# Optimization experiments

Hardware: AMD Instinct MI355X
Metric: run time of the kernel (lower is better)

The kernel has to match this reference:

```python
import jax, jax.numpy as jnp
import numpy as np

H = 512  # hidden_size


def setup_inputs() -> dict:
    key = jax.random.key(0)
    ks = jax.random.split(key, 12)
    B, E, S, V = 64, 512, 400, 50000
    s = 1.0 / np.sqrt(H)
    inp = {
        'embedded': jax.random.normal(ks[0], (B, E), jnp.float32),
        'hidden': jax.random.normal(ks[1], (1, B, H), jnp.float32),
        'encoder_states': jax.random.normal(ks[2], (S, B, H), jnp.float32),
        # GRU params (PyTorch layout: gates ordered r,z,n)
        'w_ih': jax.random.uniform(ks[3], (3 * H, E), jnp.float32, -s, s),
        'w_hh': jax.random.uniform(ks[4], (3 * H, H), jnp.float32, -s, s),
        'b_ih': jax.random.uniform(ks[5], (3 * H,), jnp.float32, -s, s),
        'b_hh': jax.random.uniform(ks[6], (3 * H,), jnp.float32, -s, s),
        # nn.Bilinear(H, H, 1)
        'bilin_w': jax.random.uniform(ks[7], (1, H, H), jnp.float32, -s, s),
        'bilin_b': jax.random.uniform(ks[8], (1,), jnp.float32, -s, s),
        # out: Linear(2H, V)
        'out_w': jax.random.uniform(ks[9], (V, 2 * H), jnp.float32, -1.0 / np.sqrt(2 * H), 1.0 / np.sqrt(2 * H)),
        'out_b': jax.random.uniform(ks[10], (V,), jnp.float32, -1.0 / np.sqrt(2 * H), 1.0 / np.sqrt(2 * H)),
    }
    return inp


def reference(embedded, hidden, encoder_states, w_ih, w_hh, b_ih, b_hh,
              bilin_w, bilin_b, out_w, out_b):
    h0 = hidden[0]                                   # [B, H]
    # --- single-step GRU cell (PyTorch gate order r, z, n) ---
    gi = embedded @ w_ih.T + b_ih                    # [B, 3H]
    gh = h0 @ w_hh.T + b_hh                          # [B, 3H]
    r = jax.nn.sigmoid(gi[:, :H] + gh[:, :H])
    z = jax.nn.sigmoid(gi[:, H:2 * H] + gh[:, H:2 * H])
    n = jnp.tanh(gi[:, 2 * H:] + r * gh[:, 2 * H:])
    h_new = (1.0 - z) * n + z * h0                   # [B, H]
    # --- bilinear attention: energy[s,b] = h_new[b] @ W @ enc[s,b] + bias ---
    tmp = h_new @ bilin_w[0]                         # [B, H]
    energy = jnp.einsum('bh,sbh->sb', tmp, encoder_states) + bilin_b[0]  # [S, B]
    attn = jax.nn.softmax(energy, axis=0)            # softmax over source positions
    context = jnp.einsum('sb,sbh->bh', attn, encoder_states)             # [B, H]
    combined = jnp.concatenate([h_new, context], axis=1)                 # [B, 2H]
    logits = combined @ out_w.T + out_b              # [B, V]
    logp = jax.nn.log_softmax(logits, axis=1)
    return logp, h_new[None], attn[:, :, None]
```

## Files before the change

### kernel.cpp

```cpp
#include <hip/hip_runtime.h>
#include <math.h>

static constexpr int H = 512;
static constexpr int B = 64;
static constexpr int FP = 8;

typedef __bf16 bf16x8 __attribute__((ext_vector_type(8)));
typedef __bf16 bf16x4 __attribute__((ext_vector_type(4)));
typedef float f32x4 __attribute__((ext_vector_type(4)));

__device__ __forceinline__ float sigmoidf_(float x) { return 1.f / (1.f + expf(-x)); }

__global__ __launch_bounds__(256) void gemm_gigh(
    const float* __restrict__ embedded, const float* __restrict__ hidden,
    const float* __restrict__ w_ih, const float* __restrict__ w_hh,
    float* __restrict__ gi, float* __restrict__ gh, int K, int N)
{
    const float* A = blockIdx.y ? hidden : embedded;
    const float* W = blockIdx.y ? w_hh : w_ih;
    float* C       = blockIdx.y ? gh : gi;

    __shared__ __bf16 As[2][64 * 64];
    __shared__ __bf16 Ws[2][64 * 64];

    const int tid  = threadIdx.x;
    const int lane = tid & 63;
    const int wv   = tid >> 6;
    const int n0   = blockIdx.x * 64;
    const int lrow = tid >> 2;
    const int lq   = tid & 3;

    const float* Aptr = A + (size_t)lrow * K + lq * 16;
    const float* Wptr = W + (size_t)(n0 + lrow) * K + lq * 16;

    f32x4 acc[4] = {};
    float4 ra[4], rw[4];
    #pragma unroll
    for (int i = 0; i < 4; ++i) {
        ra[i] = *(const float4*)(Aptr + 4 * i);
        rw[i] = *(const float4*)(Wptr + 4 * i);
    }

    const int ln = lane & 15;
    const int lk = (lane >> 4) << 3;
    const int NT = K >> 6;

    for (int t = 0; t < NT; ++t) {
        __bf16* a_s = As[t & 1];
        __bf16* w_s = Ws[t & 1];
        #pragma unroll
        for (int i = 0; i < 4; ++i) {
            const int off = ((lrow << 6) + lq * 16 + 4 * i) ^ ((lrow & 7) << 3);
            *(bf16x4*)&a_s[off] = bf16x4{ (__bf16)ra[i].x, (__bf16)ra[i].y, (__bf16)ra[i].z, (__bf16)ra[i].w };
            *(bf16x4*)&w_s[off] = bf16x4{ (__bf16)rw[i].x, (__bf16)rw[i].y, (__bf16)rw[i].z, (__bf16)rw[i].w };
        }
        __syncthreads();
        if (t + 1 < NT) {
            const float* Ap = Aptr + (t + 1) * 64;
            const float* Wp = Wptr + (t + 1) * 64;
            #pragma unroll
            for (int i = 0; i < 4; ++i) {
                ra[i] = *(const float4*)(Ap + 4 * i);
                rw[i] = *(const float4*)(Wp + 4 * i);
            }
        }
        bf16x8 bfrag[2];
        #pragma unroll
        for (int ks = 0; ks < 2; ++ks) {
            const int row = wv * 16 + ln;
            const int off = ((row << 6) + ks * 32 + lk) ^ ((row & 7) << 3);
            bfrag[ks] = *(bf16x8*)&w_s[off];
        }
        #pragma unroll
        for (int m = 0; m < 4; ++m) {
            const int row = m * 16 + ln;
            #pragma unroll
            for (int ks = 0; ks < 2; ++ks) {
                const int off = ((row << 6) + ks * 32 + lk) ^ ((row & 7) << 3);
                bf16x8 afrag = *(bf16x8*)&a_s[off];
                acc[m] = __builtin_amdgcn_mfma_f32_16x16x32_bf16(afrag, bfrag[ks], acc[m], 0, 0, 0);
            }
        }
    }

    const int col = n0 + wv * 16 + ln;
    #pragma unroll
    for (int m = 0; m < 4; ++m) {
        const int rbase = m * 16 + (lane >> 4) * 4;
        #pragma unroll
        for (int j = 0; j < 4; ++j)
            C[(size_t)(rbase + j) * N + col] = acc[m][j];
    }
}

__global__ __launch_bounds__(512) void gru_gates(
    const float* __restrict__ gi, const float* __restrict__ gh,
    const float* __restrict__ b_ih, const float* __restrict__ b_hh,
    const float* __restrict__ h0, float* __restrict__ hnew,
    __bf16* __restrict__ cbf)
{
    const int b = blockIdx.x;
    const int h = threadIdx.x;
    const size_t o = (size_t)b * 3 * H;
    const float r = sigmoidf_(gi[o + h] + gh[o + h] + b_ih[h] + b_hh[h]);
    const float z = sigmoidf_(gi[o + H + h] + gh[o + H + h] + b_ih[H + h] + b_hh[H + h]);
    const float n = tanhf(gi[o + 2 * H + h] + b_ih[2 * H + h]
                          + r * (gh[o + 2 * H + h] + b_hh[2 * H + h]));
    const float hn = (1.f - z) * n + z * h0[(size_t)b * H + h];
    hnew[(size_t)b * H + h] = hn;
    cbf[(size_t)b * 2 * H + h] = (__bf16)hn;
}

__global__ __launch_bounds__(256) void gemm_a64_kn(
    const float* __restrict__ A, const float* __restrict__ W,
    float* __restrict__ C, int K, int N, int ldc)
{
    __shared__ float As[64][68];
    __shared__ float Bs[64][68];
    const int tid = threadIdx.x;
    const int n0 = blockIdx.x * 64;
    const int tv = tid & 15;
    const int tb = tid >> 4;
    const int lrow = tid >> 2;
    const int lk0  = (tid & 3) * 16;

    float acc[4][4] = {{0.f, 0.f, 0.f, 0.f}};

    for (int kc = 0; kc < K; kc += 64) {
        #pragma unroll
        for (int i = 0; i < 4; ++i) {
            const float4 a = *(const float4*)(A + (size_t)lrow * K + kc + lk0 + 4 * i);
            As[lk0 + 4 * i + 0][lrow] = a.x;
            As[lk0 + 4 * i + 1][lrow] = a.y;
            As[lk0 + 4 * i + 2][lrow] = a.z;
            As[lk0 + 4 * i + 3][lrow] = a.w;
        }
        {
            const int v  = tid & 63;
            const int kg = tid >> 6;
            #pragma unroll
            for (int i = 0; i < 16; ++i) {
                const int kk = kg * 16 + i;
                Bs[kk][v] = (n0 + v < N) ? W[(size_t)(kc + kk) * N + n0 + v] : 0.f;
            }
        }
        __syncthreads();
        #pragma unroll 16
        for (int kk = 0; kk < 64; ++kk) {
            const float4 a = *(const float4*)&As[kk][tb * 4];
            const float4 b = *(const float4*)&Bs[kk][tv * 4];
            acc[0][0] += a.x * b.x; acc[0][1] += a.x * b.y; acc[0][2] += a.x * b.z; acc[0][3] += a.x * b.w;
            acc[1][0] += a.y * b.x; acc[1][1] += a.y * b.y; acc[1][2] += a.y * b.z; acc[1][3] += a.y * b.w;
            acc[2][0] += a.z * b.x; acc[2][1] += a.z * b.y; acc[2][2] += a.z * b.z; acc[2][3] += a.z * b.w;
            acc[3][0] += a.w * b.x; acc[3][1] += a.w * b.y; acc[3][2] += a.w * b.z; acc[3][3] += a.w * b.w;
        }
        __syncthreads();
    }
    #pragma unroll
    for (int i = 0; i < 4; ++i) {
        const int bb = tb * 4 + i;
        #pragma unroll
        for (int j = 0; j < 4; ++j) {
            const int n = n0 + tv * 4 + j;
            if (n < N) C[(size_t)bb * ldc + n] = acc[i][j];
        }
    }
}

__global__ __launch_bounds__(256) void flash4(
    const float* __restrict__ tmp, const float* __restrict__ enc,
    const float* __restrict__ bilin_b, float* __restrict__ energy,
    float* __restrict__ ctxp, float* __restrict__ mp, float* __restrict__ lp,
    int S)
{
    const int b  = blockIdx.x;
    const int p  = blockIdx.y;
    const int wv = threadIdx.x >> 6;
    const int ln = threadIdx.x & 63;
    const int chunk = (S + FP - 1) / FP;
    const int s0 = p * chunk;
    int s1 = s0 + chunk; if (s1 > S) s1 = S;
    const int k0 = ln * 8;

    const float4 t0 = *(const float4*)(tmp + (size_t)b * H + k0);
    const float4 t1 = *(const float4*)(tmp + (size_t)b * H + k0 + 4);
    const float bb = bilin_b[0];

    float m = -1e30f, l = 0.f;
    float4 c0 = {0.f, 0.f, 0.f, 0.f}, c1 = {0.f, 0.f, 0.f, 0.f};

    for (int s = s0 + wv; s < s1; s += 4) {
        const float* e = enc + ((size_t)s * B + b) * H + k0;
        const float4 e0 = *(const float4*)(e);
        const float4 e1 = *(const float4*)(e + 4);
        float d = e0.x * t0.x + e0.y * t0.y + e0.z * t0.z + e0.w * t0.w
                + e1.x * t1.x + e1.y * t1.y + e1.z * t1.z + e1.w * t1.w;
        #pragma unroll
        for (int off = 32; off; off >>= 1) d += __shfl_xor(d, off);
        const float E = d + bb;
        if (ln == 0) energy[(size_t)s * B + b] = E;
        const float mn = fmaxf(m, E);
        const float sc = expf(m - mn);
        const float w  = expf(E - mn);
        l = l * sc + w;
        c0.x = c0.x * sc + w * e0.x; c0.y = c0.y * sc + w * e0.y;
        c0.z = c0.z * sc + w * e0.z; c0.w = c0.w * sc + w * e0.w;
        c1.x = c1.x * sc + w * e1.x; c1.y = c1.y * sc + w * e1.y;
        c1.z = c1.z * sc + w * e1.z; c1.w = c1.w * sc + w * e1.w;
        m = mn;
    }

    __shared__ float sctx[4][H];
    __shared__ float sm4[4], sl4[4];
    *(float4*)&sctx[wv][k0]     = c0;
    *(float4*)&sctx[wv][k0 + 4] = c1;
    if (ln == 0) { sm4[wv] = m; sl4[wv] = l; }
    __syncthreads();
    const float bm = fmaxf(fmaxf(sm4[0], sm4[1]), fmaxf(sm4[2], sm4[3]));
    const float s0c = expf(sm4[0] - bm), s1c = expf(sm4[1] - bm);
    const float s2c = expf(sm4[2] - bm), s3c = expf(sm4[3] - bm);
    const float bl = sl4[0] * s0c + sl4[1] * s1c + sl4[2] * s2c + sl4[3] * s3c;
    for (int e = threadIdx.x; e < H; e += 256) {
        const float v = sctx[0][e] * s0c + sctx[1][e] * s1c
                      + sctx[2][e] * s2c + sctx[3][e] * s3c;
        ctxp[((size_t)b * FP + p) * H + e] = v;
    }
    if (threadIdx.x == 0) { mp[b * FP + p] = bm; lp[b * FP + p] = bl; }
}

__global__ __launch_bounds__(256) void attn_combine(
    const float* __restrict__ mp, const float* __restrict__ lp,
    const float* __restrict__ ctxp, const float* __restrict__ energy,
    __bf16* __restrict__ cbf, float* __restrict__ attn, int S)
{
    const int b = blockIdx.x;
    const int t = threadIdx.x;
    __shared__ float sc_[FP];
    __shared__ float sM, sInvL;
    if (t == 0) {
        float M = -1e30f;
        #pragma unroll
        for (int p = 0; p < FP; ++p) M = fmaxf(M, mp[b * FP + p]);
        float L = 0.f;
        #pragma unroll
        for (int p = 0; p < FP; ++p) {
            const float s = expf(mp[b * FP + p] - M);
            sc_[p] = s;
            L += lp[b * FP + p] * s;
        }
        sM = M; sInvL = 1.f / L;
    }
    __syncthreads();
    const float M = sM, invL = sInvL;

    for (int e = t; e < H; e += 256) {
        float acc = 0.f;
        #pragma unroll
        for (int p = 0; p < FP; ++p)
            acc += ctxp[((size_t)b * FP + p) * H + e] * sc_[p];
        cbf[(size_t)b * 2 * H + H + e] = (__bf16)(acc * invL);
    }
    for (int s = t; s < S; s += 256)
        attn[(size_t)s * B + b] = expf(energy[(size_t)s * B + b] - M) * invL;
}

__global__ __launch_bounds__(256) void gemm_big(
    const __bf16* __restrict__ Ab,
    const float* __restrict__ W,
    const float* __restrict__ bias,
    float* __restrict__ C, float* __restrict__ pm, float* __restrict__ ps,
    int K, int N, int ldc)
{
    __shared__ __bf16 As[64 * 256];

    const int tid  = threadIdx.x;
    const int lane = tid & 63;
    const int wv   = tid >> 6;
    const int n0   = blockIdx.x * 64 + wv * 16;
    const int ln   = lane & 15;
    const int lk8  = (lane >> 4) << 3;

    int wr = n0 + ln;
    if (wr > N - 1) wr = N - 1;
    const float* wp = W + (size_t)wr * K + lk8;

    f32x4 acc[4] = {};
    const int NQ = K >> 8;

    for (int q = 0; q < NQ; ++q) {
        __syncthreads();
        #pragma unroll
        for (int i = 0; i < 8; ++i) {
            const int c   = tid + i * 256;
            const int row = c >> 5;
            const int eb  = (c & 31) << 3;
            const bf16x8 v = *(const bf16x8*)(Ab + (size_t)row * K + q * 256 + eb);
            const int off = (row << 8) + (eb ^ ((row & 7) << 3));
            *(bf16x8*)&As[off] = v;
        }
        __syncthreads();
        #pragma unroll
        for (int ks = 0; ks < 8; ++ks) {
            const float4 w0 = *(const float4*)(wp + q * 256 + ks * 32);
            const float4 w1 = *(const float4*)(wp + q * 256 + ks * 32 + 4);
            const bf16x8 bw = { (__bf16)w0.x, (__bf16)w0.y, (__bf16)w0.z, (__bf16)w0.w,
                                (__bf16)w1.x, (__bf16)w1.y, (__bf16)w1.z, (__bf16)w1.w };
            #pragma unroll
            for (int m = 0; m < 4; ++m) {
                const int row = m * 16 + ln;
                const int off = (row << 8) + ((ks * 32 + lk8) ^ ((row & 7) << 3));
                const bf16x8 af = *(const bf16x8*)&As[off];
                acc[m] = __builtin_amdgcn_mfma_f32_16x16x32_bf16(af, bw, acc[m], 0, 0, 0);
            }
        }
    }

    const int col = n0 + ln;
    const float bv = (col < N) ? bias[col] : 0.f;
    __syncthreads();
    float* wmf = (float*)As;
    float* wsf = wmf + 256;

    #pragma unroll
    for (int m = 0; m < 4; ++m) {
        #pragma unroll
        for (int j = 0; j < 4; ++j) {
            const int rr = m * 16 + (lane >> 4) * 4 + j;
            float v = acc[m][j] + bv;
            if (col < N) C[(size_t)rr * ldc + col] = v;
            else v = -1e30f;
            float vm = v;
            #pragma unroll
            for (int off = 8; off; off >>= 1) vm = fmaxf(vm, __shfl_xor(vm, off));
            float e = (col < N) ? expf(v - vm) : 0.f;
            #pragma unroll
            for (int off = 8; off; off >>= 1) e += __shfl_xor(e, off);
            if (ln == 0) {
                wmf[wv * 64 + rr] = vm;
                wsf[wv * 64 + rr] = e;
            }
        }
    }
    __syncthreads();
    if (tid < 64) {
        const float m0 = wmf[tid], m1 = wmf[64 + tid], m2 = wmf[128 + tid], m3 = wmf[192 + tid];
        const float bm = fmaxf(fmaxf(m0, m1), fmaxf(m2, m3));
        const float bs = wsf[tid] * expf(m0 - bm) + wsf[64 + tid] * expf(m1 - bm)
                       + wsf[128 + tid] * expf(m2 - bm) + wsf[192 + tid] * expf(m3 - bm);
        pm[(size_t)tid * gridDim.x + blockIdx.x] = bm;
        ps[(size_t)tid * gridDim.x + blockIdx.x] = bs;
    }
}

__global__ __launch_bounds__(256) void lsm_rowcombine(
    const float* __restrict__ pm, const float* __restrict__ ps,
    float* __restrict__ c, int NB)
{
    const int row = blockIdx.x;
    const int t = threadIdx.x;
    const float* pmr = pm + (size_t)row * NB;
    const float* psr = ps + (size_t)row * NB;
    __shared__ float sm_[4], ss_[4];

    float m = -1e30f;
    for (int i = t; i < NB; i += 256) m = fmaxf(m, pmr[i]);
    #pragma unroll
    for (int off = 32; off; off >>= 1) m = fmaxf(m, __shfl_xor(m, off));
    if ((t & 63) == 0) sm_[t >> 6] = m;
    __syncthreads();
    m = fmaxf(fmaxf(sm_[0], sm_[1]), fmaxf(sm_[2], sm_[3]));

    float s = 0.f;
    for (int i = t; i < NB; i += 256) s += psr[i] * expf(pmr[i] - m);
    #pragma unroll
    for (int off = 32; off; off >>= 1) s += __shfl_xor(s, off);
    if ((t & 63) == 0) ss_[t >> 6] = s;
    __syncthreads();
    if (t == 0) c[row] = m + logf(ss_[0] + ss_[1] + ss_[2] + ss_[3]);
}

__global__ __launch_bounds__(256) void lsm_apply(
    float* __restrict__ logits, const float* __restrict__ c, int V)
{
    const int b = blockIdx.y;
    const int i = blockIdx.x * 256 + threadIdx.x;
    const int V4 = V >> 2;
    if (i >= V4) return;
    float4* row = (float4*)(logits + (size_t)b * V);
    float4 v = row[i];
    const float cb = c[b];
    v.x -= cb; v.y -= cb; v.z -= cb; v.w -= cb;
    row[i] = v;
}

extern "C" void kernel_launch(void* const* d_in, const int* in_sizes, int n_in,
                              void* d_out, int out_size, void* d_ws, size_t ws_size,
                              hipStream_t stream)
{
    const float* embedded = (const float*)d_in[0];
    const float* hidden   = (const float*)d_in[1];
    const float* enc      = (const float*)d_in[2];
    const float* w_ih     = (const float*)d_in[3];
    const float* w_hh     = (const float*)d_in[4];
    const float* b_ih     = (const float*)d_in[5];
    const float* b_hh     = (const float*)d_in[6];
    const float* bilin_w  = (const float*)d_in[7];
    const float* bilin_b  = (const float*)d_in[8];
    const float* out_w    = (const float*)d_in[9];
    const float* out_b    = (const float*)d_in[10];
    float* out = (float*)d_out;

    const int S = in_sizes[2] / (B * H);
    const int V = in_sizes[9] / (2 * H);
    const int NB = (V + 63) / 64;

    float* logp = out;
    float* hnew = out + (size_t)B * V;
    float* attn = hnew + (size_t)B * H;

    float* ws     = (float*)d_ws;
    float* gi     = ws;
    float* gh     = gi + (size_t)B * 3 * H;
    float* tmp    = gh + (size_t)B * 3 * H;
    float* energy = tmp + (size_t)B * H;
    float* ctxp   = energy + (size_t)S * B;
    float* mp     = ctxp + (size_t)B * FP * H;
    float* lp     = mp + (size_t)B * FP;
    float* pm     = lp + (size_t)B * FP;
    float* ps     = pm + (size_t)64 * NB;
    float* cb     = ps + (size_t)64 * NB;
    __bf16* cbf   = (__bf16*)(cb + 64);

    gemm_gigh<<<dim3(24, 2), 256, 0, stream>>>(embedded, hidden, w_ih, w_hh, gi, gh, H, 3 * H);

    gru_gates<<<B, H, 0, stream>>>(gi, gh, b_ih, b_hh, hidden, hnew, cbf);

    gemm_a64_kn<<<H / 64, 256, 0, stream>>>(hnew, bilin_w, tmp, H, H, H);

    flash4<<<dim3(B, FP), 256, 0, stream>>>(tmp, enc, bilin_b, energy, ctxp, mp, lp, S);

    attn_combine<<<B, 256, 0, stream>>>(mp, lp, ctxp, energy, cbf, attn, S);

    gemm_big<<<NB, 256, 0, stream>>>(cbf, out_w, out_b, logp, pm, ps, 2 * H, V, V);

    lsm_rowcombine<<<B, 256, 0, stream>>>(pm, ps, cb, NB);

    lsm_apply<<<dim3((V / 4 + 255) / 256, B), 256, 0, stream>>>(logp, cb, V);
}
```

Measured before the change: 153.2 us.

## Make output GEMM persistent with full A tile in LDS and register-prefetched weights

The vocabulary projection kernel becomes persistent: 256 blocks each load the entire 64x1024 bf16 activation matrix into shared memory once, then loop over output column tiles. Inside each tile the fp32 weight rows are streamed through an 8-deep register ring to keep more global loads in flight. This removes the repeated per-block staging of activations and its barriers, and aims to hide weight-load latency. In exchange it uses 128KB+ LDS per block (occupancy of one block per CU) and many more registers, so latency hiding depends entirely on in-flight loads within one block.

Result: slower. 195.9 us (+27.9%).

```diff
diff --git a/kernel.cpp b/kernel.cpp
--- a/kernel.cpp
+++ b/kernel.cpp
@@ -264,91 +264,102 @@
         attn[(size_t)s * B + b] = expf(energy[(size_t)s * B + b] - M) * invL;
 }
 
-__global__ __launch_bounds__(256) void gemm_big(
+__global__ __launch_bounds__(256, 1) void gemm_big(
     const __bf16* __restrict__ Ab,
     const float* __restrict__ W,
     const float* __restrict__ bias,
     float* __restrict__ C, float* __restrict__ pm, float* __restrict__ ps,
-    int K, int N, int ldc)
-{
-    __shared__ __bf16 As[64 * 256];
+    int N, int ldc, int NB)
+{
+    constexpr int K = 1024;
+    __shared__ __bf16 As[64 * 1024];
+    __shared__ float red[512];
 
     const int tid  = threadIdx.x;
     const int lane = tid & 63;
     const int wv   = tid >> 6;
-    const int n0   = blockIdx.x * 64 + wv * 16;
     const int ln   = lane & 15;
     const int lk8  = (lane >> 4) << 3;
 
-    int wr = n0 + ln;
-    if (wr > N - 1) wr = N - 1;
-    const float* wp = W + (size_t)wr * K + lk8;
-
-    f32x4 acc[4] = {};
-    const int NQ = K >> 8;
-
-    for (int q = 0; q < NQ; ++q) {
-        __syncthreads();
-        #pragma unroll
-        for (int i = 0; i < 8; ++i) {
-            const int c   = tid + i * 256;
-            const int row = c >> 5;
-            const int eb  = (c & 31) << 3;
-            const bf16x8 v = *(const bf16x8*)(Ab + (size_t)row * K + q * 256 + eb);
-            const int off = (row << 8) + (eb ^ ((row & 7) << 3));
-            *(bf16x8*)&As[off] = v;
-        }
-        __syncthreads();
-        #pragma unroll
-        for (int ks = 0; ks < 8; ++ks) {
-            const float4 w0 = *(const float4*)(wp + q * 256 + ks * 32);
-            const float4 w1 = *(const float4*)(wp + q * 256 + ks * 32 + 4);
+    #pragma unroll
+    for (int i = 0; i < 32; ++i) {
+        const int c   = (i << 8) + tid;
+        const int row = c >> 7;
+        const int eb  = (c & 127) << 3;
+        const bf16x8 v = *(const bf16x8*)(Ab + (size_t)row * K + eb);
+        const int off = (row << 10) + (eb ^ ((row & 7) << 3));
+        *(bf16x8*)&As[off] = v;
+    }
+    __syncthreads();
+
+    for (int t = blockIdx.x; t < NB; t += gridDim.x) {
+        const int n0 = t * 64 + wv * 16;
+        int wr = n0 + ln;
+        if (wr > N - 1) wr = N - 1;
+        const float* wq = W + (size_t)wr * K + lk8;
+
+        f32x4 acc[4] = {};
+
+        float4 ring[8][2];
+        #pragma unroll
+        for (int s = 0; s < 8; ++s) {
+            ring[s][0] = *(const float4*)(wq + s * 32);
+            ring[s][1] = *(const float4*)(wq + s * 32 + 4);
+        }
+        #pragma unroll
+        for (int s = 0; s < 32; ++s) {
+            const float4 w0 = ring[s & 7][0];
+            const float4 w1 = ring[s & 7][1];
+            if (s < 24) {
+                ring[s & 7][0] = *(const float4*)(wq + (s + 8) * 32);
+                ring[s & 7][1] = *(const float4*)(wq + (s + 8) * 32 + 4);
+            }
             const bf16x8 bw = { (__bf16)w0.x, (__bf16)w0.y, (__bf16)w0.z, (__bf16)w0.w,
                                 (__bf16)w1.x, (__bf16)w1.y, (__bf16)w1.z, (__bf16)w1.w };
             #pragma unroll
             for (int m = 0; m < 4; ++m) {
                 const int row = m * 16 + ln;
-                const int off = (row << 8) + ((ks * 32 + lk8) ^ ((row & 7) << 3));
+                const int off = (row << 10) + ((s * 32 + lk8) ^ ((row & 7) << 3));
                 const bf16x8 af = *(const bf16x8*)&As[off];
                 acc[m] = __builtin_amdgcn_mfma_f32_16x16x32_bf16(af, bw, acc[m], 0, 0, 0);
             }
         }
-    }
-
-    const int col = n0 + ln;
-    const float bv = (col < N) ? bias[col] : 0.f;
-    __syncthreads();
-    float* wmf = (float*)As;
-    float* wsf = wmf + 256;
-
-    #pragma unroll
-    for (int m = 0; m < 4; ++m) {
-        #pragma unroll
-        for (int j = 0; j < 4; ++j) {
-            const int rr = m * 16 + (lane >> 4) * 4 + j;
-            float v = acc[m][j] + bv;
-            if (col < N) C[(size_t)rr * ldc + col] = v;
-            else v = -1e30f;
-            float vm = v;
+
+        const int col = n0 + ln;
+        const float bv = (col < N) ? bias[col] : 0.f;
+        float* wmf = red;
+        float* wsf = red + 256;
+
+        #pragma unroll
+        for (int m = 0; m < 4; ++m) {
             #pragma unroll
-            for (int off = 8; off; off >>= 1) vm = fmaxf(vm, __shfl_xor(vm, off));
-            float e = (col < N) ? expf(v - vm) : 0.f;
-            #pragma unroll
-            for (int off = 8; off; off >>= 1) e += __shfl_xor(e, off);
-            if (ln == 0) {
-                wmf[wv * 64 + rr] = vm;
-                wsf[wv * 64 + rr] = e;
-            }
-        }
-    }
-    __syncthreads();
-    if (tid < 64) {
-        const float m0 = wmf[tid], m1 = wmf[64 + tid], m2 = wmf[128 + tid], m3 = wmf[192 + tid];
-        const float bm = fmaxf(fmaxf(m0, m1), fmaxf(m2, m3));
-        const float bs = wsf[tid] * expf(m0 - bm) + wsf[64 + tid] * expf(m1 - bm)
-                       + wsf[128 + tid] * expf(m2 - bm) + wsf[192 + tid] * expf(m3 - bm);
-        pm[(size_t)tid * gridDim.x + blockIdx.x] = bm;
-        ps[(size_t)tid * gridDim.x + blockIdx.x] = bs;
+            for (int j = 0; j < 4; ++j) {
+                const int rr = m * 16 + (lane >> 4) * 4 + j;
+                float v = acc[m][j] + bv;
+                if (col < N) C[(size_t)rr * ldc + col] = v;
+                else v = -1e30f;
+                float vm = v;
+                #pragma unroll
+                for (int off = 8; off; off >>= 1) vm = fmaxf(vm, __shfl_xor(vm, off));
+                float e = (col < N) ? expf(v - vm) : 0.f;
+                #pragma unroll
+                for (int off = 8; off; off >>= 1) e += __shfl_xor(e, off);
+                if (ln == 0) {
+                    wmf[wv * 64 + rr] = vm;
+                    wsf[wv * 64 + rr] = e;
+                }
+            }
+        }
+        __syncthreads();
+        if (tid < 64) {
+            const float m0 = wmf[tid], m1 = wmf[64 + tid], m2 = wmf[128 + tid], m3 = wmf[192 + tid];
+            const float bm = fmaxf(fmaxf(m0, m1), fmaxf(m2, m3));
+            const float bs = wsf[tid] * expf(m0 - bm) + wsf[64 + tid] * expf(m1 - bm)
+                           + wsf[128 + tid] * expf(m2 - bm) + wsf[192 + tid] * expf(m3 - bm);
+            pm[(size_t)tid * NB + t] = bm;
+            ps[(size_t)tid * NB + t] = bs;
+        }
+        __syncthreads();
     }
 }
 
@@ -441,7 +452,7 @@
 
     attn_combine<<<B, 256, 0, stream>>>(mp, lp, ctxp, energy, cbf, attn, S);
 
-    gemm_big<<<NB, 256, 0, stream>>>(cbf, out_w, out_b, logp, pm, ps, 2 * H, V, V);
+    gemm_big<<<256, 256, 0, stream>>>(cbf, out_w, out_b, logp, pm, ps, V, V, NB);
 
     lsm_rowcombine<<<B, 256, 0, stream>>>(pm, ps, cb, NB);
 
```

## Stream out_w and activations into LDS via async global_load_lds triple buffering

Applied to the files above, without the earlier changes.

Rewrites the large output-projection GEMM so both the fp32 weight tiles and bf16 activation tiles are copied directly into swizzled LDS with global_load_lds, using a three-stage ring buffer and manual vmcnt waits. Previously each wave read weights straight from global memory inside the MFMA loop and the activations were staged synchronously. The goal is to overlap weight streaming, which dominates this memory-bound kernel, with MFMA compute. In exchange it uses more LDS (about 76KB per block), which may lower occupancy, and it hardcodes K=1024 (4096-byte row stride, 16 phases).

After: 162.0 us. 5.7% more time.

```diff
diff --git a/kernel.cpp b/kernel.cpp
--- a/kernel.cpp
+++ b/kernel.cpp
@@ -10,6 +10,12 @@
 typedef float f32x4 __attribute__((ext_vector_type(4)));
 
 __device__ __forceinline__ float sigmoidf_(float x) { return 1.f / (1.f + expf(-x)); }
+
+__device__ __forceinline__ void gload16(const void* gsrc, void* lds) {
+    __builtin_amdgcn_global_load_lds(
+        (const __attribute__((address_space(1))) unsigned int*)gsrc,
+        (__attribute__((address_space(3))) unsigned int*)lds, 16, 0, 0);
+}
 
 __global__ __launch_bounds__(256) void gemm_gigh(
     const float* __restrict__ embedded, const float* __restrict__ hidden,
@@ -269,57 +275,82 @@
     const float* __restrict__ W,
     const float* __restrict__ bias,
     float* __restrict__ C, float* __restrict__ pm, float* __restrict__ ps,
-    int K, int N, int ldc)
-{
-    __shared__ __bf16 As[64 * 256];
+    int N, int ldc)
+{
+    __shared__ float  Wl[3][64 * 64];
+    __shared__ __bf16 Al[3][64 * 64];
+    __shared__ float  red[512];
 
     const int tid  = threadIdx.x;
     const int lane = tid & 63;
     const int wv   = tid >> 6;
-    const int n0   = blockIdx.x * 64 + wv * 16;
     const int ln   = lane & 15;
-    const int lk8  = (lane >> 4) << 3;
-
-    int wr = n0 + ln;
-    if (wr > N - 1) wr = N - 1;
-    const float* wp = W + (size_t)wr * K + lk8;
+    const int row0 = blockIdx.x * 64;
+
+    const int lane4 = lane >> 4;
+    const int g16   = lane & 15;
+    const int lane8 = lane >> 3;
+    const int g8    = lane & 7;
+    size_t wsrc[4];
+    #pragma unroll
+    for (int i = 0; i < 4; ++i) {
+        const int rl = (wv * 4 + i) * 4 + lane4;
+        int gr = row0 + rl; if (gr > N - 1) gr = N - 1;
+        wsrc[i] = (size_t)gr * 4096 + (size_t)((g16 ^ (rl & 7)) << 4);
+    }
+    size_t asrc[2];
+    #pragma unroll
+    for (int j = 0; j < 2; ++j) {
+        const int rl = (wv * 2 + j) * 8 + lane8;
+        asrc[j] = (size_t)rl * 2048 + (size_t)((g8 ^ (rl & 7)) << 4);
+    }
+    const char* wB = (const char*)W;
+    const char* aB = (const char*)Ab;
+
+    auto stage = [&](int b, int ph) {
+        #pragma unroll
+        for (int i = 0; i < 4; ++i)
+            gload16(wB + wsrc[i] + (size_t)ph * 256, &Wl[b][(wv * 4 + i) * 256]);
+        #pragma unroll
+        for (int j = 0; j < 2; ++j)
+            gload16(aB + asrc[j] + (size_t)ph * 128, &Al[b][(wv * 2 + j) * 512]);
+    };
 
     f32x4 acc[4] = {};
-    const int NQ = K >> 8;
-
-    for (int q = 0; q < NQ; ++q) {
-        __syncthreads();
-        #pragma unroll
-        for (int i = 0; i < 8; ++i) {
-            const int c   = tid + i * 256;
-            const int row = c >> 5;
-            const int eb  = (c & 31) << 3;
-            const bf16x8 v = *(const bf16x8*)(Ab + (size_t)row * K + q * 256 + eb);
-            const int off = (row << 8) + (eb ^ ((row & 7) << 3));
-            *(bf16x8*)&As[off] = v;
-        }
-        __syncthreads();
-        #pragma unroll
-        for (int ks = 0; ks < 8; ++ks) {
-            const float4 w0 = *(const float4*)(wp + q * 256 + ks * 32);
-            const float4 w1 = *(const float4*)(wp + q * 256 + ks * 32 + 4);
+
+    stage(0, 0);
+    stage(1, 1);
+
+    for (int ph = 0; ph < 16; ++ph) {
+        const int b = ph % 3;
+        if (ph + 2 < 16) stage((ph + 2) % 3, ph + 2);
+        if (ph == 15) asm volatile("s_waitcnt vmcnt(0)" ::: "memory");
+        else          asm volatile("s_waitcnt vmcnt(6)" ::: "memory");
+        __builtin_amdgcn_sched_barrier(0);
+        __builtin_amdgcn_s_barrier();
+        #pragma unroll
+        for (int ks = 0; ks < 2; ++ks) {
+            const int r  = wv * 16 + ln;
+            const int G0 = ks * 8 + (lane >> 4) * 2;
+            const float4 w0 = *(const float4*)&Wl[b][r * 64 + (((G0    ) ^ (r & 7)) << 2)];
+            const float4 w1 = *(const float4*)&Wl[b][r * 64 + (((G0 + 1) ^ (r & 7)) << 2)];
             const bf16x8 bw = { (__bf16)w0.x, (__bf16)w0.y, (__bf16)w0.z, (__bf16)w0.w,
                                 (__bf16)w1.x, (__bf16)w1.y, (__bf16)w1.z, (__bf16)w1.w };
+            const int Ga = ks * 4 + (lane >> 4);
             #pragma unroll
             for (int m = 0; m < 4; ++m) {
-                const int row = m * 16 + ln;
-                const int off = (row << 8) + ((ks * 32 + lk8) ^ ((row & 7) << 3));
-                const bf16x8 af = *(const bf16x8*)&As[off];
+                const int ar = m * 16 + ln;
+                const bf16x8 af = *(const bf16x8*)&Al[b][ar * 64 + ((Ga ^ (ar & 7)) << 3)];
                 acc[m] = __builtin_amdgcn_mfma_f32_16x16x32_bf16(af, bw, acc[m], 0, 0, 0);
             }
         }
-    }
-
-    const int col = n0 + ln;
+        __builtin_amdgcn_s_barrier();
+    }
+
+    const int col = row0 + wv * 16 + ln;
     const float bv = (col < N) ? bias[col] : 0.f;
-    __syncthreads();
-    float* wmf = (float*)As;
-    float* wsf = wmf + 256;
+    float* wmf = red;
+    float* wsf = red + 256;
 
     #pragma unroll
     for (int m = 0; m < 4; ++m) {
@@ -441,7 +472,7 @@
 
     attn_combine<<<B, 256, 0, stream>>>(mp, lp, ctxp, energy, cbf, attn, S);
 
-    gemm_big<<<NB, 256, 0, stream>>>(cbf, out_w, out_b, logp, pm, ps, 2 * H, V, V);
+    gemm_big<<<NB, 256, 0, stream>>>(cbf, out_w, out_b, logp, pm, ps, V, V);
 
     lsm_rowcombine<<<B, 256, 0, stream>>>(pm, ps, cb, NB);
 
```
